# Performance work log

Measured on AMD Instinct MI355X. Metric: run time of the kernel, lower is better.

The kernel has to match this reference:

```python
import jax, jax.numpy as jnp
import numpy as np

H = 8        # num_heads
D = 768      # d_model
DH = D // H  # d_head = 96


def setup_inputs() -> dict:
    key = jax.random.key(0)
    ks = jax.random.split(key, 12)
    B, S = 4, 2048
    s_in = 1.0 / np.sqrt(D)
    s_cat = 1.0 / np.sqrt(D)
    return {
        "input_querys": jax.random.normal(ks[0], (B, S, D), jnp.float32),
        "input_key": jax.random.normal(ks[1], (B, S, D), jnp.float32),
        "input_values": jax.random.normal(ks[2], (B, S, D), jnp.float32),
        # per-head projection weights, stacked over the head axis
        "Wq": jax.random.normal(ks[3], (H, D, DH), jnp.float32) * s_in,
        "bq": jax.random.normal(ks[4], (H, DH), jnp.float32) * s_in,
        "Wk": jax.random.normal(ks[5], (H, D, DH), jnp.float32) * s_in,
        "bk": jax.random.normal(ks[6], (H, DH), jnp.float32) * s_in,
        "Wv": jax.random.normal(ks[7], (H, D, DH), jnp.float32) * s_in,
        "bv": jax.random.normal(ks[8], (H, DH), jnp.float32) * s_in,
        # output linear: (H*DH) -> D
        "Wo": jax.random.normal(ks[9], (H * DH, D), jnp.float32) * s_cat,
        "bo": jax.random.normal(ks[10], (D,), jnp.float32) * s_cat,
    }


def reference(input_querys, input_key, input_values, Wq, bq, Wk, bk, Wv, bv, Wo, bo):
    # Per-head linear projections (vectorized over the head axis)
    # q/k/v: [B,S,D] -> [B,H,S,DH]
    Q = jnp.einsum("bsd,hdk->bhsk", input_querys, Wq) + bq[None, :, None, :]
    K = jnp.einsum("bsd,hdk->bhsk", input_key, Wk) + bk[None, :, None, :]
    V = jnp.einsum("bsd,hdk->bhsk", input_values, Wv) + bv[None, :, None, :]

    scale = 1.0 / jnp.sqrt(jnp.asarray(DH, Q.dtype))
    scores = jnp.einsum("bhsk,bhtk->bhst", Q, K) * scale  # [B,H,S,S]
    attn = jax.nn.softmax(scores, axis=-1)
    out = jnp.einsum("bhst,bhtk->bhsk", attn, V)  # [B,H,S,DH]

    # concat heads (head-major order matches torch.cat over ModuleList)
    B, _, S, _ = out.shape
    cat = out.transpose(0, 2, 1, 3).reshape(B, S, H * DH)
    return cat @ Wo + bo
```

## Files before the change

kernel.cpp:

```cpp
#include <hip/hip_runtime.h>


typedef unsigned short u16;
typedef _Float16 h16;
typedef h16 h16x8 __attribute__((ext_vector_type(8)));
typedef __fp16 fp16x2 __attribute__((ext_vector_type(2)));
typedef unsigned short u16x8 __attribute__((ext_vector_type(8)));
typedef float f32x4 __attribute__((ext_vector_type(4)));

__device__ __forceinline__ u16 f2h(float f) {
  union { h16 h; u16 u; } c; c.h = (h16)f; return c.u;
}

__global__ __launch_bounds__(256) void prep_kernel(
    const float* __restrict__ Wq, const float* __restrict__ Wk,
    const float* __restrict__ Wv, const float* __restrict__ Wo,
    u16* __restrict__ WqT, u16* __restrict__ WkT,
    u16* __restrict__ WvT, u16* __restrict__ WoT)
{
  int idx = (blockIdx.x * 256 + threadIdx.x) * 8;
  int region = idx / 589824;
  int i = idx % 589824;
  int n = i / 768;
  int d = i % 768;
  u16x8 v;
  if (region == 3) {
    #pragma unroll
    for (int j = 0; j < 8; j++) v[j] = f2h(Wo[(size_t)(d + j) * 768 + n]);
    *(u16x8*)(&WoT[i]) = v;
  } else {
    int h = n / 96, kk = n % 96;
    const float* W = (region == 0) ? Wq : (region == 1) ? Wk : Wv;
    u16* T = (region == 0) ? WqT : (region == 1) ? WkT : WvT;
    #pragma unroll
    for (int j = 0; j < 8; j++) v[j] = f2h(W[(size_t)h * 73728 + (size_t)(d + j) * 96 + kk]);
    *(u16x8*)(&T[i]) = v;
  }
}

#define GN 768
#define GK 768
#define LDA 40
#define LDB 40
#define NKT 24

template<int A_F16, int OUT_F32>
__global__ __launch_bounds__(256) void gemm_bias_kernel(
    const void* __restrict__ Av, const u16* __restrict__ BT,
    const float* __restrict__ bias, void* __restrict__ Yv)
{
  __shared__ __align__(16) u16 As[128 * LDA];
  __shared__ __align__(16) u16 Bs[64 * LDB];
  const int tid = threadIdx.x;
  const int wave = tid >> 6;
  const int lane = tid & 63;
  const int quad = lane >> 4;
  const int l16 = lane & 15;
  const int m0 = blockIdx.x * 128;
  const int n0 = blockIdx.y * 64;

  f32x4 acc[2][4];
  #pragma unroll
  for (int i = 0; i < 2; i++)
    #pragma unroll
    for (int j = 0; j < 4; j++) acc[i][j] = (f32x4){0.f, 0.f, 0.f, 0.f};

  const int ar = tid >> 2;
  const int ac = (tid & 3) * 8;

  f32x4 pf[4];
  u16x8 ph0, ph1;
  u16x8 pb;

  const u16* A16 = (const u16*)Av;
  const float* Af = (const float*)Av;

  {
    const int k0 = 0;
    if (A_F16) {
      ph0 = *(const u16x8*)(&A16[(size_t)(m0 + ar) * GK + k0 + ac]);
      ph1 = *(const u16x8*)(&A16[(size_t)(m0 + 64 + ar) * GK + k0 + ac]);
    } else {
      pf[0] = *(const f32x4*)(&Af[(size_t)(m0 + ar) * GK + k0 + ac]);
      pf[1] = *(const f32x4*)(&Af[(size_t)(m0 + ar) * GK + k0 + ac + 4]);
      pf[2] = *(const f32x4*)(&Af[(size_t)(m0 + 64 + ar) * GK + k0 + ac]);
      pf[3] = *(const f32x4*)(&Af[(size_t)(m0 + 64 + ar) * GK + k0 + ac + 4]);
    }
    pb = *(const u16x8*)(&BT[(size_t)(n0 + ar) * GK + k0 + ac]);
  }

  for (int kt = 0; kt < NKT; kt++) {
    if (A_F16) {
      *(u16x8*)(&As[ar * LDA + ac]) = ph0;
      *(u16x8*)(&As[(64 + ar) * LDA + ac]) = ph1;
    } else {
      u16x8 h0, h1;
      #pragma unroll
      for (int j = 0; j < 4; j++) {
        h0[j] = f2h(pf[0][j]); h0[4 + j] = f2h(pf[1][j]);
        h1[j] = f2h(pf[2][j]); h1[4 + j] = f2h(pf[3][j]);
      }
      *(u16x8*)(&As[ar * LDA + ac]) = h0;
      *(u16x8*)(&As[(64 + ar) * LDA + ac]) = h1;
    }
    *(u16x8*)(&Bs[ar * LDB + ac]) = pb;
    __syncthreads();

    if (kt + 1 < NKT) {
      const int k0 = (kt + 1) * 32;
      if (A_F16) {
        ph0 = *(const u16x8*)(&A16[(size_t)(m0 + ar) * GK + k0 + ac]);
        ph1 = *(const u16x8*)(&A16[(size_t)(m0 + 64 + ar) * GK + k0 + ac]);
      } else {
        pf[0] = *(const f32x4*)(&Af[(size_t)(m0 + ar) * GK + k0 + ac]);
        pf[1] = *(const f32x4*)(&Af[(size_t)(m0 + ar) * GK + k0 + ac + 4]);
        pf[2] = *(const f32x4*)(&Af[(size_t)(m0 + 64 + ar) * GK + k0 + ac]);
        pf[3] = *(const f32x4*)(&Af[(size_t)(m0 + 64 + ar) * GK + k0 + ac + 4]);
      }
      pb = *(const u16x8*)(&BT[(size_t)(n0 + ar) * GK + k0 + ac]);
    }

    h16x8 af[2], bfr[4];
    #pragma unroll
    for (int mf = 0; mf < 2; mf++)
      af[mf] = *(const h16x8*)(&As[(wave * 32 + mf * 16 + l16) * LDA + quad * 8]);
    #pragma unroll
    for (int nf = 0; nf < 4; nf++)
      bfr[nf] = *(const h16x8*)(&Bs[(nf * 16 + l16) * LDB + quad * 8]);
    #pragma unroll
    for (int mf = 0; mf < 2; mf++)
      #pragma unroll
      for (int nf = 0; nf < 4; nf++)
        acc[mf][nf] = __builtin_amdgcn_mfma_f32_16x16x32_f16(af[mf], bfr[nf], acc[mf][nf], 0, 0, 0);

    if (kt + 1 < NKT) __syncthreads();
  }

  #pragma unroll
  for (int nf = 0; nf < 4; nf++) {
    const int n = n0 + nf * 16 + l16;
    const float bv = bias[n];
    #pragma unroll
    for (int mf = 0; mf < 2; mf++)
      #pragma unroll
      for (int r = 0; r < 4; r++) {
        const int m = m0 + wave * 32 + mf * 16 + quad * 4 + r;
        const float val = acc[mf][nf][r] + bv;
        if (OUT_F32) ((float*)Yv)[(size_t)m * GN + n] = val;
        else         ((u16*)Yv)[(size_t)m * GN + n] = f2h(val);
      }
  }
}

#define SEQ 2048
#define LQK 104
#define LVT 72
#define LPS 72

__global__ __launch_bounds__(512, 4) void attn_kernel(
    const u16* __restrict__ Q, const u16* __restrict__ K,
    const u16* __restrict__ V, u16* __restrict__ O)
{
  __shared__ __align__(16) u16 Ks[64 * LQK];
  __shared__ __align__(16) u16 Vt[96 * LVT];
  __shared__ __align__(16) u16 Ps[8][16 * LPS];

  const int tid = threadIdx.x;
  const int wave = tid >> 6;
  const int lane = tid & 63;
  const int quad = lane >> 4;
  const int l16 = lane & 15;

  const int bh = blockIdx.y;
  const int b = bh >> 3, h = bh & 7;
  const int q0 = blockIdx.x * 128;

  const size_t batch_off = (size_t)b * SEQ * 768;
  const u16* Kb0 = K + batch_off + h * 96;
  const u16* Vb0 = V + batch_off + h * 96;

  h16x8 qf[3];
  {
    const u16* Qrow = Q + batch_off + (size_t)(q0 + wave * 16 + l16) * 768 + h * 96 + quad * 8;
    #pragma unroll
    for (int ks = 0; ks < 3; ks++)
      qf[ks] = *(const h16x8*)(&Qrow[ks * 32]);
  }

  f32x4 o[6];
  #pragma unroll
  for (int i = 0; i < 6; i++) o[i] = (f32x4){0.f, 0.f, 0.f, 0.f};
  float m_raw = -1e30f;
  float lrow = 0.f;

  const float sc = 0.14724498f;

  const int tg = tid & 7;
  const int dg = tid >> 3;

  u16* Pw = &Ps[wave][0];

  for (int kt = 0; kt < SEQ / 64; kt++) {
    __syncthreads();
    const u16* Kb = Kb0 + (size_t)kt * 64 * 768;
    const u16* Vb = Vb0 + (size_t)kt * 64 * 768;
    {
      int i = tid;
      int r = i / 12, c = i % 12;
      *(u16x8*)(&Ks[r * LQK + c * 8]) = *(const u16x8*)(&Kb[(size_t)r * 768 + c * 8]);
      i = tid + 512;
      if (i < 768) {
        r = i / 12; c = i % 12;
        *(u16x8*)(&Ks[r * LQK + c * 8]) = *(const u16x8*)(&Kb[(size_t)r * 768 + c * 8]);
      }
    }
    if (tid < 96) {
      const u16* src = Vb + (size_t)(tg * 8) * 768 + dg * 8;
      u16x8 tin[8];
      #pragma unroll
      for (int i = 0; i < 8; i++) tin[i] = *(const u16x8*)(&src[(size_t)i * 768]);
      #pragma unroll
      for (int j = 0; j < 8; j++) {
        u16x8 t;
        #pragma unroll
        for (int i = 0; i < 8; i++) t[i] = tin[i][j];
        *(u16x8*)(&Vt[(dg * 8 + j) * LVT + tg * 8]) = t;
      }
    }
    __syncthreads();

    f32x4 s[4];
    #pragma unroll
    for (int kf = 0; kf < 4; kf++) s[kf] = (f32x4){0.f, 0.f, 0.f, 0.f};
    #pragma unroll
    for (int ks = 0; ks < 3; ks++) {
      #pragma unroll
      for (int kf = 0; kf < 4; kf++) {
        h16x8 a = *(const h16x8*)(&Ks[(kf * 16 + l16) * LQK + ks * 32 + quad * 8]);
        s[kf] = __builtin_amdgcn_mfma_f32_16x16x32_f16(a, qf[ks], s[kf], 0, 0, 0);
      }
    }

    float mx = s[0][0];
    #pragma unroll
    for (int kf = 0; kf < 4; kf++)
      #pragma unroll
      for (int r = 0; r < 4; r++) mx = fmaxf(mx, s[kf][r]);
    mx = fmaxf(mx, __shfl_xor(mx, 16));
    mx = fmaxf(mx, __shfl_xor(mx, 32));
    float mnew = fmaxf(m_raw, mx);
    float alpha = exp2f(sc * (m_raw - mnew));
    m_raw = mnew;
    const float c0 = sc * mnew;
    float ps = 0.f;
    #pragma unroll
    for (int kf = 0; kf < 4; kf++)
      #pragma unroll
      for (int r = 0; r < 4; r++) {
        float p = exp2f(fmaf(s[kf][r], sc, -c0));
        s[kf][r] = p;
        ps += p;
      }
    ps += __shfl_xor(ps, 16);
    ps += __shfl_xor(ps, 32);
    lrow = lrow * alpha + ps;
    #pragma unroll
    for (int nfo = 0; nfo < 6; nfo++)
      #pragma unroll
      for (int r = 0; r < 4; r++) o[nfo][r] *= alpha;

    #pragma unroll
    for (int kf = 0; kf < 4; kf++)
      #pragma unroll
      for (int rp = 0; rp < 4; rp += 2) {
        fp16x2 pk = __builtin_amdgcn_cvt_pkrtz(s[kf][rp], s[kf][rp + 1]);
        *(fp16x2*)(&Pw[l16 * LPS + kf * 16 + quad * 4 + rp]) = pk;
      }

    #pragma unroll
    for (int ks = 0; ks < 2; ks++) {
      h16x8 pfr = *(const h16x8*)(&Pw[l16 * LPS + ks * 32 + quad * 8]);
      #pragma unroll
      for (int nfo = 0; nfo < 6; nfo++) {
        h16x8 vfr = *(const h16x8*)(&Vt[(nfo * 16 + l16) * LVT + ks * 32 + quad * 8]);
        o[nfo] = __builtin_amdgcn_mfma_f32_16x16x32_f16(vfr, pfr, o[nfo], 0, 0, 0);
      }
    }
  }

  const float inv = 1.0f / lrow;
  u16* Ob = O + batch_off + (size_t)(q0 + wave * 16 + l16) * 768 + h * 96;
  #pragma unroll
  for (int nfo = 0; nfo < 6; nfo++) {
    fp16x2 lo = __builtin_amdgcn_cvt_pkrtz(o[nfo][0] * inv, o[nfo][1] * inv);
    fp16x2 hi = __builtin_amdgcn_cvt_pkrtz(o[nfo][2] * inv, o[nfo][3] * inv);
    *(fp16x2*)(&Ob[nfo * 16 + quad * 4]) = lo;
    *(fp16x2*)(&Ob[nfo * 16 + quad * 4 + 2]) = hi;
  }
}

extern "C" void kernel_launch(void* const* d_in, const int* in_sizes, int n_in,
                              void* d_out, int out_size, void* d_ws, size_t ws_size,
                              hipStream_t stream) {
  const float* Xq = (const float*)d_in[0];
  const float* Xk = (const float*)d_in[1];
  const float* Xv = (const float*)d_in[2];
  const float* Wq = (const float*)d_in[3];
  const float* bq = (const float*)d_in[4];
  const float* Wk = (const float*)d_in[5];
  const float* bk = (const float*)d_in[6];
  const float* Wv = (const float*)d_in[7];
  const float* bv = (const float*)d_in[8];
  const float* Wo = (const float*)d_in[9];
  const float* bo = (const float*)d_in[10];
  float* out = (float*)d_out;

  u16* outu = (u16*)d_out;
  u16* Vb  = outu;
  u16* WqT = outu + 6291456;
  u16* WkT = WqT + 589824;
  u16* WvT = WkT + 589824;
  u16* WoT = (u16*)d_ws;

  u16* Kb = (u16*)d_in[2];
  u16* Qb = (u16*)d_in[1];
  u16* Ab = (u16*)d_in[0];

  prep_kernel<<<1152, 256, 0, stream>>>(Wq, Wk, Wv, Wo, WqT, WkT, WvT, WoT);
  dim3 ggrid(64, 12);
  gemm_bias_kernel<0, 0><<<ggrid, 256, 0, stream>>>(Xv, WvT, bv, Vb);
  gemm_bias_kernel<0, 0><<<ggrid, 256, 0, stream>>>(Xk, WkT, bk, Kb);
  gemm_bias_kernel<0, 0><<<ggrid, 256, 0, stream>>>(Xq, WqT, bq, Qb);
  attn_kernel<<<dim3(16, 32), 512, 0, stream>>>(Qb, Kb, Vb, Ab);
  gemm_bias_kernel<1, 1><<<ggrid, 256, 0, stream>>>(Ab, WoT, bo, out);
}
```

Baseline: 335.1 us.

## Pre-convert inputs to fp16, use direct-to-LDS GEMM loads, pre-transposed V, conditional rescale

```diff
diff --git a/kernel.cpp b/kernel.cpp
--- a/kernel.cpp
+++ b/kernel.cpp
@@ -6,10 +6,29 @@
 typedef h16 h16x8 __attribute__((ext_vector_type(8)));
 typedef __fp16 fp16x2 __attribute__((ext_vector_type(2)));
 typedef unsigned short u16x8 __attribute__((ext_vector_type(8)));
+typedef unsigned short u16x4 __attribute__((ext_vector_type(4)));
 typedef float f32x4 __attribute__((ext_vector_type(4)));
 
 __device__ __forceinline__ u16 f2h(float f) {
   union { h16 h; u16 u; } c; c.h = (h16)f; return c.u;
+}
+
+__device__ __forceinline__ void gll16(const void* g, void* l) {
+  __builtin_amdgcn_global_load_lds(
+      (const __attribute__((address_space(1))) void*)g,
+      (__attribute__((address_space(3))) void*)l, 16, 0, 0);
+}
+
+__global__ __launch_bounds__(256) void cvt_kernel(
+    const float* __restrict__ X, u16* __restrict__ Y)
+{
+  int i = (blockIdx.x * 256 + threadIdx.x) * 8;
+  f32x4 a = *(const f32x4*)(X + i);
+  f32x4 b = *(const f32x4*)(X + i + 4);
+  u16x8 hv;
+  #pragma unroll
+  for (int j = 0; j < 4; j++) { hv[j] = f2h(a[j]); hv[4 + j] = f2h(b[j]); }
+  *(u16x8*)(Y + i) = hv;
 }
 
 __global__ __launch_bounds__(256) void prep_kernel(
@@ -38,19 +57,15 @@
   }
 }
 
-#define GN 768
 #define GK 768
-#define LDA 40
-#define LDB 40
-#define NKT 24
-
-template<int A_F16, int OUT_F32>
-__global__ __launch_bounds__(256) void gemm_bias_kernel(
-    const void* __restrict__ Av, const u16* __restrict__ BT,
+
+template<int OUT_MODE>
+__global__ __launch_bounds__(256) void gemm16(
+    const u16* __restrict__ A, const u16* __restrict__ BT,
     const float* __restrict__ bias, void* __restrict__ Yv)
 {
-  __shared__ __align__(16) u16 As[128 * LDA];
-  __shared__ __align__(16) u16 Bs[64 * LDB];
+  __shared__ __align__(16) u16 As[128 * 32];
+  __shared__ __align__(16) u16 Bs[64 * 32];
   const int tid = threadIdx.x;
   const int wave = tid >> 6;
   const int lane = tid & 63;
@@ -65,75 +80,34 @@
     #pragma unroll
     for (int j = 0; j < 4; j++) acc[i][j] = (f32x4){0.f, 0.f, 0.f, 0.f};
 
-  const int ar = tid >> 2;
-  const int ac = (tid & 3) * 8;
-
-  f32x4 pf[4];
-  u16x8 ph0, ph1;
-  u16x8 pb;
-
-  const u16* A16 = (const u16*)Av;
-  const float* Af = (const float*)Av;
-
-  {
-    const int k0 = 0;
-    if (A_F16) {
-      ph0 = *(const u16x8*)(&A16[(size_t)(m0 + ar) * GK + k0 + ac]);
-      ph1 = *(const u16x8*)(&A16[(size_t)(m0 + 64 + ar) * GK + k0 + ac]);
-    } else {
-      pf[0] = *(const f32x4*)(&Af[(size_t)(m0 + ar) * GK + k0 + ac]);
-      pf[1] = *(const f32x4*)(&Af[(size_t)(m0 + ar) * GK + k0 + ac + 4]);
-      pf[2] = *(const f32x4*)(&Af[(size_t)(m0 + 64 + ar) * GK + k0 + ac]);
-      pf[3] = *(const f32x4*)(&Af[(size_t)(m0 + 64 + ar) * GK + k0 + ac + 4]);
-    }
-    pb = *(const u16x8*)(&BT[(size_t)(n0 + ar) * GK + k0 + ac]);
-  }
-
-  for (int kt = 0; kt < NKT; kt++) {
-    if (A_F16) {
-      *(u16x8*)(&As[ar * LDA + ac]) = ph0;
-      *(u16x8*)(&As[(64 + ar) * LDA + ac]) = ph1;
-    } else {
-      u16x8 h0, h1;
-      #pragma unroll
-      for (int j = 0; j < 4; j++) {
-        h0[j] = f2h(pf[0][j]); h0[4 + j] = f2h(pf[1][j]);
-        h1[j] = f2h(pf[2][j]); h1[4 + j] = f2h(pf[3][j]);
-      }
-      *(u16x8*)(&As[ar * LDA + ac]) = h0;
-      *(u16x8*)(&As[(64 + ar) * LDA + ac]) = h1;
-    }
-    *(u16x8*)(&Bs[ar * LDB + ac]) = pb;
+  const int Lr = lane >> 2, Lc = (lane & 3) * 8;
+  const u16* gA0 = A + (size_t)(m0 + wave * 32 + Lr) * GK + Lc;
+  const u16* gA1 = gA0 + (size_t)16 * GK;
+  const u16* gB  = BT + (size_t)(n0 + wave * 16 + Lr) * GK + Lc;
+  u16* lA0 = &As[(wave * 32) * 32];
+  u16* lA1 = &As[(wave * 32 + 16) * 32];
+  u16* lB  = &Bs[(wave * 16) * 32];
+
+  for (int kt = 0; kt < 24; kt++) {
+    gll16(gA0, lA0);
+    gll16(gA1, lA1);
+    gll16(gB, lB);
+    gA0 += 32; gA1 += 32; gB += 32;
     __syncthreads();
 
-    if (kt + 1 < NKT) {
-      const int k0 = (kt + 1) * 32;
-      if (A_F16) {
-        ph0 = *(const u16x8*)(&A16[(size_t)(m0 + ar) * GK + k0 + ac]);
-        ph1 = *(const u16x8*)(&A16[(size_t)(m0 + 64 + ar) * GK + k0 + ac]);
-      } else {
-        pf[0] = *(const f32x4*)(&Af[(size_t)(m0 + ar) * GK + k0 + ac]);
-        pf[1] = *(const f32x4*)(&Af[(size_t)(m0 + ar) * GK + k0 + ac + 4]);
-        pf[2] = *(const f32x4*)(&Af[(size_t)(m0 + 64 + ar) * GK + k0 + ac]);
-        pf[3] = *(const f32x4*)(&Af[(size_t)(m0 + 64 + ar) * GK + k0 + ac + 4]);
-      }
-      pb = *(const u16x8*)(&BT[(size_t)(n0 + ar) * GK + k0 + ac]);
-    }
-
-    h16x8 af[2], bfr[4];
+    h16x8 af[2], bf[4];
     #pragma unroll
     for (int mf = 0; mf < 2; mf++)
-      af[mf] = *(const h16x8*)(&As[(wave * 32 + mf * 16 + l16) * LDA + quad * 8]);
+      af[mf] = *(const h16x8*)(&As[(wave * 32 + mf * 16 + l16) * 32 + quad * 8]);
     #pragma unroll
     for (int nf = 0; nf < 4; nf++)
-      bfr[nf] = *(const h16x8*)(&Bs[(nf * 16 + l16) * LDB + quad * 8]);
+      bf[nf] = *(const h16x8*)(&Bs[(nf * 16 + l16) * 32 + quad * 8]);
     #pragma unroll
     for (int mf = 0; mf < 2; mf++)
       #pragma unroll
       for (int nf = 0; nf < 4; nf++)
-        acc[mf][nf] = __builtin_amdgcn_mfma_f32_16x16x32_f16(af[mf], bfr[nf], acc[mf][nf], 0, 0, 0);
-
-    if (kt + 1 < NKT) __syncthreads();
+        acc[mf][nf] = __builtin_amdgcn_mfma_f32_16x16x32_f16(af[mf], bf[nf], acc[mf][nf], 0, 0, 0);
+    __syncthreads();
   }
 
   #pragma unroll
@@ -141,14 +115,23 @@
     const int n = n0 + nf * 16 + l16;
     const float bv = bias[n];
     #pragma unroll
-    for (int mf = 0; mf < 2; mf++)
-      #pragma unroll
-      for (int r = 0; r < 4; r++) {
-        const int m = m0 + wave * 32 + mf * 16 + quad * 4 + r;
-        const float val = acc[mf][nf][r] + bv;
-        if (OUT_F32) ((float*)Yv)[(size_t)m * GN + n] = val;
-        else         ((u16*)Yv)[(size_t)m * GN + n] = f2h(val);
-      }
+    for (int mf = 0; mf < 2; mf++) {
+      const int m = m0 + wave * 32 + mf * 16 + quad * 4;
+      if (OUT_MODE == 2) {
+        const int b = m >> 11, s = m & 2047;
+        u16x4 pk;
+        #pragma unroll
+        for (int r = 0; r < 4; r++) pk[r] = f2h(acc[mf][nf][r] + bv);
+        *(u16x4*)(&((u16*)Yv)[(size_t)b * 768 * 2048 + (size_t)n * 2048 + s]) = pk;
+      } else {
+        #pragma unroll
+        for (int r = 0; r < 4; r++) {
+          const float val = acc[mf][nf][r] + bv;
+          if (OUT_MODE == 1) ((float*)Yv)[(size_t)(m + r) * GK + n] = val;
+          else               ((u16*)Yv)[(size_t)(m + r) * GK + n] = f2h(val);
+        }
+      }
+    }
   }
 }
 
@@ -159,7 +142,7 @@
 
 __global__ __launch_bounds__(512, 4) void attn_kernel(
     const u16* __restrict__ Q, const u16* __restrict__ K,
-    const u16* __restrict__ V, u16* __restrict__ O)
+    const u16* __restrict__ VT, u16* __restrict__ O)
 {
   __shared__ __align__(16) u16 Ks[64 * LQK];
   __shared__ __align__(16) u16 Vt[96 * LVT];
@@ -176,58 +159,57 @@
   const int q0 = blockIdx.x * 128;
 
   const size_t batch_off = (size_t)b * SEQ * 768;
-  const u16* Kb0 = K + batch_off + h * 96;
-  const u16* Vb0 = V + batch_off + h * 96;
+  const u16* Kg = K + batch_off + h * 96;
+  const u16* Vg = VT + (size_t)b * 768 * 2048 + (size_t)(h * 96) * 2048;
 
   h16x8 qf[3];
   {
     const u16* Qrow = Q + batch_off + (size_t)(q0 + wave * 16 + l16) * 768 + h * 96 + quad * 8;
     #pragma unroll
-    for (int ks = 0; ks < 3; ks++)
-      qf[ks] = *(const h16x8*)(&Qrow[ks * 32]);
-  }
+    for (int ks = 0; ks < 3; ks++) qf[ks] = *(const h16x8*)(&Qrow[ks * 32]);
+  }
+
+  const int kr0 = tid / 12, kc0 = (tid % 12) * 8;
+  const int kr1 = (tid + 512) / 12, kc1 = ((tid + 512) % 12) * 8;
+  const int vr0 = tid >> 3, vc0 = (tid & 7) * 8;
+  const int vr1 = (tid + 512) >> 3, vc1 = ((tid + 512) & 7) * 8;
+  const bool extra = tid < 256;
 
   f32x4 o[6];
   #pragma unroll
   for (int i = 0; i < 6; i++) o[i] = (f32x4){0.f, 0.f, 0.f, 0.f};
-  float m_raw = -1e30f;
-  float lrow = 0.f;
-
+  float m_raw = -1e30f, lrow = 0.f;
   const float sc = 0.14724498f;
 
-  const int tg = tid & 7;
-  const int dg = tid >> 3;
-
   u16* Pw = &Ps[wave][0];
 
+  u16x8 kA, kB, vA, vB;
+  kA = *(const u16x8*)(&Kg[(size_t)kr0 * 768 + kc0]);
+  vA = *(const u16x8*)(&Vg[(size_t)vr0 * 2048 + vc0]);
+  if (extra) {
+    kB = *(const u16x8*)(&Kg[(size_t)kr1 * 768 + kc1]);
+    vB = *(const u16x8*)(&Vg[(size_t)vr1 * 2048 + vc1]);
+  }
+
   for (int kt = 0; kt < SEQ / 64; kt++) {
+    *(u16x8*)(&Ks[kr0 * LQK + kc0]) = kA;
+    *(u16x8*)(&Vt[vr0 * LVT + vc0]) = vA;
+    if (extra) {
+      *(u16x8*)(&Ks[kr1 * LQK + kc1]) = kB;
+      *(u16x8*)(&Vt[vr1 * LVT + vc1]) = vB;
+    }
     __syncthreads();
-    const u16* Kb = Kb0 + (size_t)kt * 64 * 768;
-    const u16* Vb = Vb0 + (size_t)kt * 64 * 768;
-    {
-      int i = tid;
-      int r = i / 12, c = i % 12;
-      *(u16x8*)(&Ks[r * LQK + c * 8]) = *(const u16x8*)(&Kb[(size_t)r * 768 + c * 8]);
-      i = tid + 512;
-      if (i < 768) {
-        r = i / 12; c = i % 12;
-        *(u16x8*)(&Ks[r * LQK + c * 8]) = *(const u16x8*)(&Kb[(size_t)r * 768 + c * 8]);
-      }
-    }
-    if (tid < 96) {
-      const u16* src = Vb + (size_t)(tg * 8) * 768 + dg * 8;
-      u16x8 tin[8];
-      #pragma unroll
-      for (int i = 0; i < 8; i++) tin[i] = *(const u16x8*)(&src[(size_t)i * 768]);
-      #pragma unroll
-      for (int j = 0; j < 8; j++) {
-        u16x8 t;
-        #pragma unroll
-        for (int i = 0; i < 8; i++) t[i] = tin[i][j];
-        *(u16x8*)(&Vt[(dg * 8 + j) * LVT + tg * 8]) = t;
-      }
-    }
-    __syncthreads();
+
+    if (kt + 1 < SEQ / 64) {
+      const u16* Kn = Kg + (size_t)(kt + 1) * 64 * 768;
+      const u16* Vn = Vg + (size_t)(kt + 1) * 64;
+      kA = *(const u16x8*)(&Kn[(size_t)kr0 * 768 + kc0]);
+      vA = *(const u16x8*)(&Vn[(size_t)vr0 * 2048 + vc0]);
+      if (extra) {
+        kB = *(const u16x8*)(&Kn[(size_t)kr1 * 768 + kc1]);
+        vB = *(const u16x8*)(&Vn[(size_t)vr1 * 2048 + vc1]);
+      }
+    }
 
     f32x4 s[4];
     #pragma unroll
@@ -248,10 +230,9 @@
       for (int r = 0; r < 4; r++) mx = fmaxf(mx, s[kf][r]);
     mx = fmaxf(mx, __shfl_xor(mx, 16));
     mx = fmaxf(mx, __shfl_xor(mx, 32));
-    float mnew = fmaxf(m_raw, mx);
-    float alpha = exp2f(sc * (m_raw - mnew));
-    m_raw = mnew;
-    const float c0 = sc * mnew;
+    const float mold = m_raw;
+    m_raw = fmaxf(mold, mx);
+    const float c0 = sc * m_raw;
     float ps = 0.f;
     #pragma unroll
     for (int kf = 0; kf < 4; kf++)
@@ -263,11 +244,15 @@
       }
     ps += __shfl_xor(ps, 16);
     ps += __shfl_xor(ps, 32);
-    lrow = lrow * alpha + ps;
-    #pragma unroll
-    for (int nfo = 0; nfo < 6; nfo++)
-      #pragma unroll
-      for (int r = 0; r < 4; r++) o[nfo][r] *= alpha;
+    if (__any(m_raw > mold)) {
+      const float alpha = exp2f(sc * (mold - m_raw));
+      lrow *= alpha;
+      #pragma unroll
+      for (int nfo = 0; nfo < 6; nfo++)
+        #pragma unroll
+        for (int r = 0; r < 4; r++) o[nfo][r] *= alpha;
+    }
+    lrow += ps;
 
     #pragma unroll
     for (int kf = 0; kf < 4; kf++)
@@ -286,6 +271,7 @@
         o[nfo] = __builtin_amdgcn_mfma_f32_16x16x32_f16(vfr, pfr, o[nfo], 0, 0, 0);
       }
     }
+    __syncthreads();
   }
 
   const float inv = 1.0f / lrow;
@@ -313,24 +299,28 @@
   const float* bv = (const float*)d_in[8];
   const float* Wo = (const float*)d_in[9];
   const float* bo = (const float*)d_in[10];
-  float* out = (float*)d_out;
 
   u16* outu = (u16*)d_out;
-  u16* Vb  = outu;
-  u16* WqT = outu + 6291456;
-  u16* WkT = WqT + 589824;
-  u16* WvT = WkT + 589824;
+  u16* outA = outu;
+  u16* outB = outu + 6291456;
+  u16* WqT = outB;
+  u16* WkT = outB + 589824;
+  u16* WvT = outB + 1179648;
   u16* WoT = (u16*)d_ws;
 
-  u16* Kb = (u16*)d_in[2];
-  u16* Qb = (u16*)d_in[1];
-  u16* Ab = (u16*)d_in[0];
-
+  u16* VTb = (u16*)d_in[2];
+  u16* K16 = (u16*)d_in[1];
+  u16* Q16 = (u16*)d_in[0];
+  u16* A16 = (u16*)d_in[0] + 6291456;
+
+  dim3 ggrid(64, 12);
   prep_kernel<<<1152, 256, 0, stream>>>(Wq, Wk, Wv, Wo, WqT, WkT, WvT, WoT);
-  dim3 ggrid(64, 12);
-  gemm_bias_kernel<0, 0><<<ggrid, 256, 0, stream>>>(Xv, WvT, bv, Vb);
-  gemm_bias_kernel<0, 0><<<ggrid, 256, 0, stream>>>(Xk, WkT, bk, Kb);
-  gemm_bias_kernel<0, 0><<<ggrid, 256, 0, stream>>>(Xq, WqT, bq, Qb);
-  attn_kernel<<<dim3(16, 32), 512, 0, stream>>>(Qb, Kb, Vb, Ab);
-  gemm_bias_kernel<1, 1><<<ggrid, 256, 0, stream>>>(Ab, WoT, bo, out);
-}
+  cvt_kernel<<<3072, 256, 0, stream>>>(Xv, outA);
+  gemm16<2><<<ggrid, 256, 0, stream>>>(outA, WvT, bv, VTb);
+  cvt_kernel<<<3072, 256, 0, stream>>>(Xk, outA);
+  gemm16<0><<<ggrid, 256, 0, stream>>>(outA, WkT, bk, K16);
+  cvt_kernel<<<3072, 256, 0, stream>>>(Xq, outA);
+  gemm16<0><<<ggrid, 256, 0, stream>>>(outA, WqT, bq, Q16);
+  attn_kernel<<<dim3(16, 32), 512, 0, stream>>>(Q16, K16, VTb, A16);
+  gemm16<1><<<ggrid, 256, 0, stream>>>(A16, WoT, bo, (float*)d_out);
+}
```

After: 315.3 us. 5.9% less time.
